# Kernel tuning notes

Hardware: AMD Instinct MI355X
Metric: run time of the kernel (lower is better)

Reference implementation:

```python
import jax, jax.numpy as jnp
import numpy as np

N, C, L = 1024, 3, 6000
CONV_CH = [20, 32, 64, 20]
K = 3            # conv kernel size, padding (K-1)//2 = 1 -> SAME
POOL = 2
HID = 100
FLAT_DIM = (L // POOL**4 + 2 * C + 1) * CONV_CH[-1]  # (375 + 7) * 20 = 7640


def setup_inputs() -> dict:
    key = jax.random.key(0)
    ks = jax.random.split(key, 10)
    d = {"x": jax.random.normal(ks[0], (N, C, L), jnp.float32)}
    ins = [C] + CONV_CH[:-1]
    for i, (ic, oc) in enumerate(zip(ins, CONV_CH)):
        d[f"w{i}"] = jax.random.normal(ks[1 + i], (oc, ic, K), jnp.float32) * (1.0 / np.sqrt(ic * K))
        d[f"b{i}"] = jnp.zeros((oc,), jnp.float32)
    d["wc"] = jax.random.normal(ks[6], (CONV_CH[-1], C, 1), jnp.float32) * (1.0 / np.sqrt(C))
    d["bc"] = jnp.zeros((CONV_CH[-1],), jnp.float32)
    d["wl0"] = jax.random.normal(ks[7], (HID, FLAT_DIM), jnp.float32) * (1.0 / np.sqrt(FLAT_DIM))
    d["bl0"] = jnp.zeros((HID,), jnp.float32)
    d["wl1"] = jax.random.normal(ks[8], (2, HID), jnp.float32) * (1.0 / np.sqrt(HID))
    d["bl1"] = jnp.zeros((2,), jnp.float32)
    return d


def conv1d(x, w, b, pad):
    # x: (N, C_in, L), w: (C_out, C_in, K)
    out = jax.lax.conv_general_dilated(x, w, (1,), [(pad, pad)],
                                       dimension_numbers=('NCH', 'OIH', 'NCH'))
    return out + b[None, :, None]


def maxpool2(x):
    n, c, l = x.shape  # l always even here (6000 / 2^k)
    return x.reshape(n, c, l // 2, 2).max(-1)


def cov_eig_feats(x):
    # batched covariance as a single contraction (avoids the O(N*L*C*C) bmm intermediate)
    n, c, l = x.shape
    diff = x - x.mean(-1, keepdims=True)
    cov = jnp.einsum('ncl,ndl->ncd', diff, diff) / (l - 1)  # (N, C, C)
    # cov is symmetric PSD -> eigh (real); torch uses generic eig and keeps real parts
    vals, vecs = jnp.linalg.eigh(cov)
    vals = vals[..., None] / vals.max()          # global max over batch, like torch
    cov = cov / jnp.abs(cov).max()
    return jnp.concatenate([cov, vals, vecs], axis=-1)  # (N, C, 2C+1)


def reference(x, w0, b0, w1, b1, w2, b2, w3, b3, wc, bc, wl0, bl0, wl1, bl1):
    feats = jax.lax.stop_gradient(cov_eig_feats(x))  # torch branch is @no_grad
    h = x
    for w, b in ((w0, b0), (w1, b1), (w2, b2), (w3, b3)):
        h = maxpool2(jax.nn.relu(conv1d(h, w, b, (K - 1) // 2)))
    h = h.reshape(h.shape[0], -1)                    # (N, 20*375)
    h1 = jax.nn.relu(conv1d(feats, wc, bc, 0))       # (N, 20, 7)
    h1 = h1.reshape(h1.shape[0], -1)
    h = jnp.concatenate([h, h1], axis=1)             # (N, 7640)
    h = jax.nn.relu(h @ wl0.T + bl0)
    out = h @ wl1.T + bl1                            # (N, 2)
    return (out[:, :1], out[:, 1:])
```

## Files before the change

kernel.cpp:

```cpp
#include <hip/hip_runtime.h>
#include <hip/hip_bf16.h>
#include <hip/hip_fp16.h>
#include <math.h>

#define NBATCH 1024
#define LIN    6000
#define HCATW  7640
#define HID    100

#define TCH   54
#define NCHK  7

#define ASZ 3552
#define BSZ 4460

#define W0OFF 0
#define W1OFF 192
#define W2OFF 1472
#define W3OFF 5568
#define B0OFF 9664
#define B1OFF 9684
#define B2OFF 9716
#define B3OFF 9780
#define WREPSZ 9800

#define WL0HSZ (HID * (HCATW/2))

#define FCNS 8

typedef _Float16 v2h __attribute__((ext_vector_type(2)));

__device__ __forceinline__ float fdot2_f16(unsigned int a, unsigned int b, float c) {
#if __has_builtin(__builtin_amdgcn_fdot2)
    v2h ah, bh;
    __builtin_memcpy(&ah, &a, 4);
    __builtin_memcpy(&bh, &b, 4);
    return __builtin_amdgcn_fdot2(ah, bh, c, false);
#else
    float d;
    asm("v_dot2_f32_f16 %0, %1, %2, %3" : "=v"(d) : "v"(a), "v"(b), "v"(c));
    return d;
#endif
}

__device__ __forceinline__ void pack_one(int idx, int OC, int IC, int OCG,
                                         int OPG, int WSTR,
                                         const float* __restrict__ w,
                                         float* __restrict__ dst)
{
    if (idx >= OCG * IC * WSTR) return;
    int ocg = idx / (IC * WSTR);
    int r   = idx - ocg * (IC * WSTR);
    int ic  = r / WSTR;
    int q   = r - ic * WSTR;
    int o   = q / 3, k = q - o * 3;
    int oc  = ocg * OPG + o;
    dst[idx] = (o < OPG && oc < OC) ? w[(oc * IC + ic) * 3 + k] : 0.f;
}

__device__ __forceinline__ void pack_pk(int idx, int OC, int IC, int OCG, int OPG,
                                        const float* __restrict__ w,
                                        unsigned int* __restrict__ dst)
{
    if (idx >= OCG * IC * 16) return;
    int ocg = idx / (IC * 16);
    int r   = idx - ocg * (IC * 16);
    int ic  = r >> 4, q = r & 15;
    int o   = q & 7;
    int oc  = ocg * OPG + o;
    bool valid = (o < OPG) && (oc < OC);
    unsigned int v = 0;
    if (valid) {
        const float* ws = w + (oc * IC + ic) * 3;
        if (q < 8) {
            unsigned int lo = __half_as_ushort(__float2half(ws[0]));
            unsigned int hi = __half_as_ushort(__float2half(ws[1]));
            v = lo | (hi << 16);
        } else {
            v = __float_as_uint(ws[2]);
        }
    }
    dst[idx] = v;
}

__global__ __launch_bounds__(256) void repack_kernel(
    const float* __restrict__ w0, const float* __restrict__ b0,
    const float* __restrict__ w1, const float* __restrict__ b1,
    const float* __restrict__ w2, const float* __restrict__ b2,
    const float* __restrict__ w3, const float* __restrict__ b3,
    float* __restrict__ wrep)
{
    int idx = blockIdx.x * 256 + threadIdx.x;
    unsigned int* wu = (unsigned int*)wrep;
    pack_one(idx, 20,  3, 4, 5, 16, w0, wrep + W0OFF);
    pack_pk (idx, 32, 20, 4, 8, w1, wu + W1OFF);
    pack_pk (idx, 64, 32, 8, 8, w2, wu + W2OFF);
    pack_pk (idx, 20, 64, 4, 5, w3, wu + W3OFF);
    if (idx < 20)            wrep[B0OFF + idx] = b0[idx];
    else if (idx < 52)  { int i = idx - 20;  wrep[B1OFF + i] = b1[i]; }
    else if (idx < 116) { int i = idx - 52;  wrep[B2OFF + i] = b2[i]; }
    else if (idx < 136) { int i = idx - 116; wrep[B3OFF + i] = b3[i]; }
}

__global__ __launch_bounds__(256) void wl0h_kernel(const float* __restrict__ wl0,
                                                   unsigned int* __restrict__ wl0h)
{
    int idx = blockIdx.x * 256 + threadIdx.x;
    if (idx >= WL0HSZ) return;
    float a = wl0[idx * 2], b = wl0[idx * 2 + 1];
    unsigned int lo = __half_as_ushort(__float2half(a));
    unsigned int hi = __half_as_ushort(__float2half(b));
    wl0h[idx] = lo | (hi << 16);
}

template<int IC, int OC, int OCG, int OPG, int WSTR, int JOUT, int LG, int JBLK,
         bool IN16, bool OUT16, bool PKW, bool FINAL>
__device__ __forceinline__ void stage_eo(const float* __restrict__ in,
                                         float* __restrict__ out,
                                         float* __restrict__ outg,
                                         const float* __restrict__ wrep,
                                         const float* __restrict__ brep,
                                         int pbase, int o3, int wv, int lane,
                                         int zero)
{
    constexpr int PIN  = JOUT + 1;
    constexpr int POUT = JOUT / 2;
    constexpr int NJT  = (JOUT + 64 * JBLK - 1) / (64 * JBLK);
    for (int task = wv; task < OCG * NJT; task += 8) {
        const int ocg = task / NJT;
        const int jt  = task - ocg * NJT;
        const int j0  = jt * (64 * JBLK) + lane;
        const float* bp = brep + ocg * OPG;
        float ae[JBLK][OPG], ao[JBLK][OPG];
#pragma unroll
        for (int t = 0; t < JBLK; ++t)
#pragma unroll
            for (int o = 0; o < OPG; ++o) { ae[t][o] = bp[o]; ao[t][o] = ae[t][o]; }
        const float* wbase = wrep + ocg * (IC * WSTR) + zero;
#pragma unroll 2
        for (int ic = 0; ic < IC; ++ic) {
            const float* wp = wbase + ic * WSTR;
            float wr[WSTR];
#pragma unroll
            for (int q = 0; q < WSTR / 4; ++q)
                *(float4*)&wr[q * 4] = *(const float4*)(wp + q * 4);
#pragma unroll
            for (int t = 0; t < JBLK; ++t) {
                const int jj = j0 + t * 64;
                const int jc = (jj < JOUT) ? jj : (JOUT - 1);
                if constexpr (PKW) {
                    const float* ipw = in + ic * PIN;
                    uint2 pw;
                    __builtin_memcpy(&pw, ipw + jc, 8);
                    const unsigned int crossu = (pw.x >> 16) | (pw.y << 16);
                    v2h h1; __builtin_memcpy(&h1, &pw.y, 4);
                    const float e1 = (float)h1.x, o1 = (float)h1.y;
#pragma unroll
                    for (int o = 0; o < OPG; ++o) {
                        const unsigned int wpk = __float_as_uint(wr[o]);
                        const float w2 = wr[8 + o];
                        ae[t][o] = fdot2_f16(pw.x,  wpk, ae[t][o]);
                        ao[t][o] = fdot2_f16(crossu, wpk, ao[t][o]);
                        ae[t][o] = fmaf(e1, w2, ae[t][o]);
                        ao[t][o] = fmaf(o1, w2, ao[t][o]);
                    }
                } else {
                    float e0, e1, o0, o1;
                    if constexpr (IN16) {
                        const float* ipw = in + ic * PIN;
                        uint2 pw;
                        __builtin_memcpy(&pw, ipw + jc, 8);
                        __half2 h0 = *reinterpret_cast<const __half2*>(&pw.x);
                        __half2 h1 = *reinterpret_cast<const __half2*>(&pw.y);
                        e0 = __low2float(h0); o0 = __high2float(h0);
                        e1 = __low2float(h1); o1 = __high2float(h1);
                    } else {
                        const float* ip = in + ic * (2 * PIN);
                        float2 ev, ov;
                        __builtin_memcpy(&ev, ip + jc, 8);
                        __builtin_memcpy(&ov, ip + PIN + jc, 8);
                        e0 = ev.x; e1 = ev.y;
                        o0 = ov.x; o1 = ov.y;
                    }
#pragma unroll
                    for (int o = 0; o < OPG; ++o) {
                        const float w0 = wr[o*3+0], w1 = wr[o*3+1], w2 = wr[o*3+2];
                        ae[t][o] = fmaf(e0, w0, fmaf(o0, w1, fmaf(e1, w2, ae[t][o])));
                        ao[t][o] = fmaf(o0, w0, fmaf(e1, w1, fmaf(o1, w2, ao[t][o])));
                    }
                }
            }
        }
#pragma unroll
        for (int t = 0; t < JBLK; ++t) {
            const int jj = j0 + t * 64;
            if constexpr (FINAL) {
                const int gj = o3 + jj;
                if (gj < 375 && jj < JOUT) {
#pragma unroll
                    for (int o = 0; o < OPG; ++o)
                        outg[(ocg*OPG+o) * 375 + gj] =
                            fmaxf(fmaxf(ae[t][o], ao[t][o]), 0.f);
                }
            } else {
                const int g = pbase + jj;
                const bool val = (jj < JOUT) && (g >= 0) && (g < LG);
                if (jj < JOUT) {
                    if constexpr (OUT16) {
                        __half* dh = (__half*)out;
#pragma unroll
                        for (int o = 0; o < OPG; ++o) {
                            float v = val ? fmaxf(fmaxf(ae[t][o], ao[t][o]), 0.f)
                                          : 0.f;
                            dh[(ocg*OPG+o) * JOUT + jj] = __float2half(v);
                        }
                    } else {
                        float* dst = out + ((jj & 1) ? POUT : 0) + (jj >> 1);
#pragma unroll
                        for (int o = 0; o < OPG; ++o)
                            dst[(ocg*OPG+o) * JOUT] =
                                val ? fmaxf(fmaxf(ae[t][o], ao[t][o]), 0.f) : 0.f;
                    }
                }
            }
        }
    }
}

__device__ __forceinline__ void stage3_split(const float* __restrict__ in,
                                             float* __restrict__ part,
                                             float* __restrict__ outg,
                                             const float* __restrict__ wrep,
                                             const float* __restrict__ brep,
                                             int o3, int wv, int lane, int zero)
{
    constexpr int JOUT = 54, PIND = 55, OPG = 5, WSTR = 16;
    const int ocg = wv & 3, ih = wv >> 2;
    const int j  = lane;
    const int jc = (j < JOUT) ? j : (JOUT - 1);
    const float* bp = brep + ocg * OPG;
    float ae[OPG], ao[OPG];
#pragma unroll
    for (int o = 0; o < OPG; ++o) {
        float b = ih ? 0.f : bp[o];
        ae[o] = b; ao[o] = b;
    }
    const float* wbase = wrep + (ocg * 64 + ih * 32) * WSTR + zero;
#pragma unroll 2
    for (int ic = 0; ic < 32; ++ic) {
        const float* ipw = in + (ih * 32 + ic) * PIND;
        uint2 pw;
        __builtin_memcpy(&pw, ipw + jc, 8);
        const unsigned int crossu = (pw.x >> 16) | (pw.y << 16);
        v2h h1; __builtin_memcpy(&h1, &pw.y, 4);
        const float e1 = (float)h1.x, o1 = (float)h1.y;
        const float* wp = wbase + ic * WSTR;
        float wr[WSTR];
#pragma unroll
        for (int q = 0; q < WSTR / 4; ++q)
            *(float4*)&wr[q * 4] = *(const float4*)(wp + q * 4);
#pragma unroll
        for (int o = 0; o < OPG; ++o) {
            const unsigned int wpk = __float_as_uint(wr[o]);
            const float w2 = wr[8 + o];
            ae[o] = fdot2_f16(pw.x,   wpk, ae[o]);
            ao[o] = fdot2_f16(crossu, wpk, ao[o]);
            ae[o] = fmaf(e1, w2, ae[o]);
            ao[o] = fmaf(o1, w2, ao[o]);
        }
    }
    if (ih == 1) {
#pragma unroll
        for (int o = 0; o < OPG; ++o) {
            float2 p = make_float2(ae[o], ao[o]);
            __builtin_memcpy(part + (ocg * OPG + o) * 128 + lane * 2, &p, 8);
        }
    }
    __syncthreads();
    if (ih == 0) {
#pragma unroll
        for (int o = 0; o < OPG; ++o) {
            float2 p;
            __builtin_memcpy(&p, part + (ocg * OPG + o) * 128 + lane * 2, 8);
            ae[o] += p.x; ao[o] += p.y;
        }
        const int gj = o3 + j;
        if (gj < 375 && j < JOUT) {
#pragma unroll
            for (int o = 0; o < OPG; ++o)
                outg[(ocg * OPG + o) * 375 + gj] =
                    fmaxf(fmaxf(ae[o], ao[o]), 0.f);
        }
    }
}

__global__ __launch_bounds__(512, 8) void conv_chain_eo(
    const float* __restrict__ x,
    const float* __restrict__ wrep,
    float* __restrict__ hcat)
{
    __shared__ float A[ASZ];
    __shared__ float B[BSZ];

    const int tid  = threadIdx.x;
    const int wv   = __builtin_amdgcn_readfirstlane(tid >> 6);
    const int lane = tid & 63;
    const int zero = __builtin_amdgcn_ds_bpermute(0, 0);
    const int n     = blockIdx.x / NCHK;
    const int chunk = blockIdx.x % NCHK;
    const int o3 = chunk * TCH;
    const int p2 = 2*o3 - 1, p1 = 4*o3 - 3, p0 = 8*o3 - 7, xs = 16*o3 - 15;

    const float* xn = x + (size_t)n * 3 * LIN;
    for (int idx = tid; idx < 3 * 894; idx += 512) {
        int c = idx / 894, i = idx - c * 894;
        int g = xs + i;
        float v = (g >= 0 && g < LIN) ? xn[c * LIN + g] : 0.f;
        A[c * 894 + ((i & 1) ? 447 : 0) + (i >> 1)] = v;
    }
    __syncthreads();
    stage_eo< 3, 20, 4, 5, 16, 446, 3000, 2, false, true,  false, false>(
        A, B, nullptr, wrep + W0OFF, wrep + B0OFF, p0, o3, wv, lane, zero);
    __syncthreads();
    stage_eo<20, 32, 4, 8, 16, 222, 1500, 2, true,  true,  true,  false>(
        B, A, nullptr, wrep + W1OFF, wrep + B1OFF, p1, o3, wv, lane, zero);
    __syncthreads();
    stage_eo<32, 64, 8, 8, 16, 110,  750, 2, true,  true,  true,  false>(
        A, B, nullptr, wrep + W2OFF, wrep + B2OFF, p2, o3, wv, lane, zero);
    __syncthreads();
    stage3_split(B, A, hcat + (size_t)n * HCATW,
                 wrep + W3OFF, wrep + B3OFF, o3, wv, lane, zero);
}

__device__ __forceinline__ float fsign(float a, float b) {
    return (b >= 0.0f) ? fabsf(a) : -fabsf(a);
}
__device__ __forceinline__ float slapy2(float xx, float yy) {
    float xa = fabsf(xx), ya = fabsf(yy);
    float w = fmaxf(xa, ya), z = fminf(xa, ya);
    if (z == 0.f) return w;
    float t = z / w;
    return w * sqrtf(1.f + t*t);
}
__device__ __forceinline__ void slartg(float f, float g, float& c, float& s, float& r) {
    if (g == 0.f)      { c = 1.f; s = 0.f; r = f; }
    else if (f == 0.f) { c = 0.f; s = (g >= 0.f ? 1.f : -1.f); r = fabsf(g); }
    else {
        float d = sqrtf(f*f + g*g);
        c = fabsf(f) / d;
        r = fsign(d, f);
        s = g / r;
    }
}
__device__ void slaev2(float a, float b, float cc,
                       float& rt1, float& rt2, float& cs1, float& sn1) {
    float sm = a + cc, df = a - cc;
    float adf = fabsf(df);
    float tb = b + b, ab = fabsf(tb);
    float acmx, acmn;
    if (fabsf(a) > fabsf(cc)) { acmx = a; acmn = cc; } else { acmx = cc; acmn = a; }
    float rt;
    if (adf > ab)      { float t = ab/adf; rt = adf*sqrtf(1.f + t*t); }
    else if (adf < ab) { float t = adf/ab; rt = ab*sqrtf(1.f + t*t); }
    else rt = ab * sqrtf(2.f);
    int sgn1;
    if (sm < 0.f)      { rt1 = 0.5f*(sm - rt); sgn1 = -1; rt2 = (acmx/rt1)*acmn - (b/rt1)*b; }
    else if (sm > 0.f) { rt1 = 0.5f*(sm + rt); sgn1 =  1; rt2 = (acmx/rt1)*acmn - (b/rt1)*b; }
    else               { rt1 = 0.5f*rt; rt2 = -0.5f*rt; sgn1 = 1; }
    float cs; int sgn2;
    if (df >= 0.f) { cs = df + rt; sgn2 = 1; } else { cs = df - rt; sgn2 = -1; }
    float acs = fabsf(cs);
    if (acs > ab) {
        float ct = -tb / cs;
        sn1 = 1.f / sqrtf(1.f + ct*ct);
        cs1 = ct * sn1;
    } else {
        if (ab == 0.f) { cs1 = 1.f; sn1 = 0.f; }
        else {
            float tn = -cs / tb;
            cs1 = 1.f / sqrtf(1.f + tn*tn);
            sn1 = tn * cs1;
        }
    }
    if (sgn1 == sgn2) { float tn = cs1; cs1 = -sn1; sn1 = tn; }
}
__device__ __forceinline__ void rot_cols(float z[3][3], int jc, float c, float s) {
    for (int i = 0; i < 3; ++i) {
        float t = z[i][jc+1];
        z[i][jc+1] = c*t - s*z[i][jc];
        z[i][jc]   = s*t + c*z[i][jc];
    }
}

__device__ void ssteqr3(float d[3], float e[2], float z[3][3]) {
    const float eps    = 5.9604645e-8f;
    const float eps2   = eps * eps;
    const float safmin = 1.17549435e-38f;
    const int n = 3;
    for (int i = 0; i < 3; ++i)
        for (int j = 0; j < 3; ++j) z[i][j] = (i == j) ? 1.f : 0.f;
    const int nmaxit = n * 30;
    int jtot = 0;
    float cw[2], sw[2];
    int l1 = 1, l, m, lend, lsv, lendsv;

L10:
    if (l1 > n) goto L160;
    if (l1 > 1) e[l1-2] = 0.f;
    if (l1 <= n-1) {
        for (m = l1; m <= n-1; ++m) {
            float tst = fabsf(e[m-1]);
            if (tst == 0.f) goto L30;
            if (tst <= (sqrtf(fabsf(d[m-1])) * sqrtf(fabsf(d[m]))) * eps) {
                e[m-1] = 0.f;
                goto L30;
            }
        }
    }
    m = n;
L30:
    l = l1; lsv = l; lend = m; lendsv = lend; l1 = m + 1;
    if (lend == l) goto L10;
    if (fabsf(d[lend-1]) < fabsf(d[l-1])) { lend = lsv; l = lendsv; }
    if (lend > l) {
L40:
        if (l != lend) {
            bool found = false;
            for (m = l; m <= lend-1; ++m) {
                float tst = e[m-1]*e[m-1];
                if (tst <= (eps2*fabsf(d[m-1]))*fabsf(d[m]) + safmin) { found = true; break; }
            }
            if (!found) m = lend;
        } else m = lend;
        if (m < lend) e[m-1] = 0.f;
        {
            float p = d[l-1];
            if (m == l) {
                d[l-1] = p;
                l = l + 1;
                if (l <= lend) goto L40;
                goto L140;
            }
            if (m == l+1) {
                float rt1, rt2, c2, s2;
                slaev2(d[l-1], e[l-1], d[l], rt1, rt2, c2, s2);
                rot_cols(z, l-1, c2, s2);
                d[l-1] = rt1; d[l] = rt2; e[l-1] = 0.f;
                l += 2;
                if (l <= lend) goto L40;
                goto L140;
            }
            if (jtot == nmaxit) goto L140;
            jtot++;
            float g = (d[l] - p) / (2.f * e[l-1]);
            float r = slapy2(g, 1.f);
            g = d[m-1] - p + e[l-1] / (g + fsign(r, g));
            float s = 1.f, c = 1.f;
            p = 0.f;
            for (int i = m-1; i >= l; --i) {
                float f = s * e[i-1];
                float b = c * e[i-1];
                slartg(g, f, c, s, r);
                if (i != m-1) e[i] = r;
                g = d[i] - p;
                r = (d[i-1] - g)*s + 2.f*c*b;
                p = s * r;
                d[i] = g + p;
                g = c*r - b;
                cw[i-l] = c; sw[i-l] = -s;
            }
            for (int jj = m-l; jj >= 1; --jj)
                rot_cols(z, l + jj - 2, cw[jj-1], sw[jj-1]);
            d[l-1] = d[l-1] - p;
            e[l-1] = g;
            goto L40;
        }
    } else {
L90:
        if (l != lend) {
            bool found = false;
            for (m = l; m >= lend+1; --m) {
                float tst = e[m-2]*e[m-2];
                if (tst <= (eps2*fabsf(d[m-1]))*fabsf(d[m-2]) + safmin) { found = true; break; }
            }
            if (!found) m = lend;
        } else m = lend;
        if (m > lend) e[m-2] = 0.f;
        {
            float p = d[l-1];
            if (m == l) {
                d[l-1] = p;
                l = l - 1;
                if (l >= lend) goto L90;
                goto L140;
            }
            if (m == l-1) {
                float rt1, rt2, c2, s2;
                slaev2(d[l-2], e[l-2], d[l-1], rt1, rt2, c2, s2);
                rot_cols(z, l-2, c2, s2);
                d[l-2] = rt1; d[l-1] = rt2; e[l-2] = 0.f;
                l -= 2;
                if (l >= lend) goto L90;
                goto L140;
            }
            if (jtot == nmaxit) goto L140;
            jtot++;
            float g = (d[l-2] - p) / (2.f * e[l-2]);
            float r = slapy2(g, 1.f);
            g = d[m-1] - p + e[l-2] / (g + fsign(r, g));
            float s = 1.f, c = 1.f;
            p = 0.f;
            for (int i = m; i <= l-1; ++i) {
                float f = s * e[i-1];
                float b = c * e[i-1];
                slartg(g, f, c, s, r);
                if (i != m) e[i-2] = r;
                g = d[i-1] - p;
                r = (d[i] - g)*s + 2.f*c*b;
                p = s * r;
                d[i-1] = g + p;
                g = c*r - b;
                cw[i-m] = c; sw[i-m] = s;
            }
            for (int jj = 1; jj <= l-m; ++jj)
                rot_cols(z, m + jj - 2, cw[jj-1], sw[jj-1]);
            d[l-1] = d[l-1] - p;
            e[l-2] = g;
            goto L90;
        }
    }
L140:
    if (jtot < nmaxit) goto L10;
L160:
    for (int ii = 2; ii <= n; ++ii) {
        int i = ii - 1, k = i;
        float p = d[i-1];
        for (int j = ii; j <= n; ++j)
            if (d[j-1] < p) { k = j; p = d[j-1]; }
        if (k != i) {
            d[k-1] = d[i-1]; d[i-1] = p;
            for (int r0 = 0; r0 < 3; ++r0) {
                float t = z[r0][i-1]; z[r0][i-1] = z[r0][k-1]; z[r0][k-1] = t;
            }
        }
    }
}

__global__ __launch_bounds__(256) void cov_eig_kernel(const float* __restrict__ x,
                                                      float* __restrict__ eigbuf,
                                                      unsigned int* __restrict__ gmax)
{
    __shared__ float part[4][9];
    const int n = blockIdx.x;
    const float* xn = x + (size_t)n * 3 * LIN;
    float v[9] = {0,0,0,0,0,0,0,0,0};
    for (int l = threadIdx.x; l < LIN; l += 256) {
        float a = xn[l], b = xn[LIN + l], c = xn[2*LIN + l];
        v[0] += a; v[1] += b; v[2] += c;
        v[3] = fmaf(a,a,v[3]); v[4] = fmaf(a,b,v[4]); v[5] = fmaf(a,c,v[5]);
        v[6] = fmaf(b,b,v[6]); v[7] = fmaf(b,c,v[7]); v[8] = fmaf(c,c,v[8]);
    }
#pragma unroll
    for (int off = 32; off > 0; off >>= 1)
#pragma unroll
        for (int i = 0; i < 9; ++i) v[i] += __shfl_down(v[i], off, 64);
    const int wv = threadIdx.x >> 6, lane = threadIdx.x & 63;
    if (lane == 0)
        for (int i = 0; i < 9; ++i) part[wv][i] = v[i];
    __syncthreads();
    if (threadIdx.x == 0) {
        float t[9];
        for (int i = 0; i < 9; ++i)
            t[i] = part[0][i] + part[1][i] + part[2][i] + part[3][i];
        const float Lf = (float)LIN;
        float m0 = t[0]/Lf, m1 = t[1]/Lf, m2 = t[2]/Lf;
        float c00 = (t[3] - Lf*m0*m0) / (Lf - 1.f);
        float c01 = (t[4] - Lf*m0*m1) / (Lf - 1.f);
        float c02 = (t[5] - Lf*m0*m2) / (Lf - 1.f);
        float c11 = (t[6] - Lf*m1*m1) / (Lf - 1.f);
        float c12 = (t[7] - Lf*m1*m2) / (Lf - 1.f);
        float c22 = (t[8] - Lf*m2*m2) / (Lf - 1.f);

        float dd[3], ee[2], tau, v2;
        {
            float a21 = c01, a31 = c02, a22 = c11, a32 = c12, a33 = c22;
            float xnorm = fabsf(a31);
            if (xnorm == 0.f) {
                tau = 0.f; v2 = 0.f;
                dd[0] = c00; dd[1] = a22; dd[2] = a33;
                ee[0] = a21; ee[1] = a32;
            } else {
                float beta = -fsign(slapy2(a21, xnorm), a21);
                tau = (beta - a21) / beta;
                v2  = a31 / (a21 - beta);
                ee[0] = beta;
                float x1 = tau*(a22 + a32*v2);
                float x2 = tau*(a32 + a33*v2);
                float al = -0.5f*tau*(x1 + x2*v2);
                float w1 = x1 + al;
                float w2 = x2 + al*v2;
                a22 -= 2.f*w1;
                a32 -= (v2*w1 + w2);
                a33 -= 2.f*v2*w2;
                dd[0] = c00; dd[1] = a22; dd[2] = a33;
                ee[1] = a32;
            }
        }
        float zz[3][3];
        ssteqr3(dd, ee, zz);
        if (tau != 0.f) {
            for (int j = 0; j < 3; ++j) {
                float sum = zz[1][j] + v2*zz[2][j];
                zz[1][j] -= tau * sum;
                zz[2][j] -= tau * v2 * sum;
            }
        }

        float* eb = eigbuf + n * 21;
        eb[0] = c00; eb[1] = c01; eb[2] = c02;
        eb[3] = c01; eb[4] = c11; eb[5] = c12;
        eb[6] = c02; eb[7] = c12; eb[8] = c22;
        eb[9] = dd[0]; eb[10] = dd[1]; eb[11] = dd[2];
        for (int c = 0; c < 3; ++c)
            for (int k = 0; k < 3; ++k) eb[12 + c*3 + k] = zz[c][k];

        float vmax = fmaxf(dd[0], fmaxf(dd[1], dd[2]));
        float cmax = 0.f;
        for (int i = 0; i < 9; ++i) cmax = fmaxf(cmax, fabsf(eb[i]));
        atomicMax(&gmax[0], __float_as_uint(vmax));
        atomicMax(&gmax[1], __float_as_uint(cmax));
    }
}

__global__ __launch_bounds__(256) void feats_kernel(const float* __restrict__ eigbuf,
                                                    const unsigned int* __restrict__ gmax,
                                                    const float* __restrict__ wc,
                                                    const float* __restrict__ bc,
                                                    float* __restrict__ hcat)
{
    const int n = blockIdx.x;
    const int t = threadIdx.x;
    if (t >= 140) return;
    const int o = t / 7, j = t % 7;
    const float* eb = eigbuf + n * 21;
    const float vmax = __uint_as_float(gmax[0]);
    const float cmax = __uint_as_float(gmax[1]);
    float f0, f1, f2;
    if (j < 3)       { f0 = eb[0*3+j]/cmax; f1 = eb[1*3+j]/cmax; f2 = eb[2*3+j]/cmax; }
    else if (j == 3) { f0 = eb[9]/vmax;     f1 = eb[10]/vmax;    f2 = eb[11]/vmax; }
    else             { int k = j-4; f0 = eb[12+0*3+k]; f1 = eb[12+1*3+k]; f2 = eb[12+2*3+k]; }
    float r = bc[o] + wc[o*3+0]*f0 + wc[o*3+1]*f1 + wc[o*3+2]*f2;
    hcat[(size_t)n*HCATW + 7500 + o*7 + j] = fmaxf(r, 0.f);
}

__global__ __launch_bounds__(512) void fc01_kernel(const float* __restrict__ hcat,
                                                   const unsigned int* __restrict__ wl0h,
                                                   const float* __restrict__ bl0,
                                                   const float* __restrict__ wl1,
                                                   const float* __restrict__ bl1,
                                                   float* __restrict__ out)
{
    __shared__ __half hl[FCNS * HCATW];
    __shared__ float hbuf[FCNS * HID];
    const int tid = threadIdx.x;
    const int n0 = blockIdx.x * FCNS;
    for (int i = tid; i < FCNS * (HCATW/4); i += 512) {
        int s  = i / (HCATW/4);
        int k4 = i - s * (HCATW/4);
        float4 v = *(const float4*)(hcat + (size_t)(n0 + s) * HCATW + k4 * 4);
        __half2 h01 = __floats2half2_rn(v.x, v.y);
        __half2 h23 = __floats2half2_rn(v.z, v.w);
        *(__half2*)(hl + s * HCATW + k4 * 4)     = h01;
        *(__half2*)(hl + s * HCATW + k4 * 4 + 2) = h23;
    }
    __syncthreads();
    const int wv = tid >> 6;
    const int lane = tid & 63;
    for (int ot = wv; ot < HID / 4; ot += 8) {
        float acc[4][FCNS];
#pragma unroll
        for (int oo = 0; oo < 4; ++oo)
#pragma unroll
            for (int s = 0; s < FCNS; ++s) acc[oo][s] = 0.f;
        for (int k = lane * 8; k < HCATW; k += 512) {
            uint4 hv[FCNS];
#pragma unroll
            for (int s = 0; s < FCNS; ++s)
                hv[s] = *(const uint4*)(hl + s * HCATW + k);
#pragma unroll
            for (int oo = 0; oo < 4; ++oo) {
                const uint4 wp = *(const uint4*)(wl0h + (ot*4+oo) * (HCATW/2) + (k >> 1));
#pragma unroll
                for (int s = 0; s < FCNS; ++s) {
                    float a = acc[oo][s];
                    a = fdot2_f16(hv[s].x, wp.x, a);
                    a = fdot2_f16(hv[s].y, wp.y, a);
                    a = fdot2_f16(hv[s].z, wp.z, a);
                    a = fdot2_f16(hv[s].w, wp.w, a);
                    acc[oo][s] = a;
                }
            }
        }
#pragma unroll
        for (int off = 32; off > 0; off >>= 1)
#pragma unroll
            for (int oo = 0; oo < 4; ++oo)
#pragma unroll
                for (int s = 0; s < FCNS; ++s)
                    acc[oo][s] += __shfl_down(acc[oo][s], off, 64);
        if (lane == 0) {
#pragma unroll
            for (int oo = 0; oo < 4; ++oo) {
                const float b = bl0[ot*4+oo];
#pragma unroll
                for (int s = 0; s < FCNS; ++s)
                    hbuf[s * HID + ot*4+oo] = fmaxf(acc[oo][s] + b, 0.f);
            }
        }
    }
    __syncthreads();
    if (tid < 2 * FCNS) {
        const int s = tid >> 1, r = tid & 1;
        const float* w = wl1 + r * HID;
        float acc = bl1[r];
        for (int k = 0; k < HID; ++k) acc = fmaf(hbuf[s * HID + k], w[k], acc);
        out[r * NBATCH + n0 + s] = acc;
    }
}

extern "C" void kernel_launch(void* const* d_in, const int* in_sizes, int n_in,
                              void* d_out, int out_size, void* d_ws, size_t ws_size,
                              hipStream_t stream)
{
    const float* x   = (const float*)d_in[0];
    const float* w0  = (const float*)d_in[1];
    const float* b0  = (const float*)d_in[2];
    const float* w1  = (const float*)d_in[3];
    const float* b1  = (const float*)d_in[4];
    const float* w2  = (const float*)d_in[5];
    const float* b2  = (const float*)d_in[6];
    const float* w3  = (const float*)d_in[7];
    const float* b3  = (const float*)d_in[8];
    const float* wc  = (const float*)d_in[9];
    const float* bc  = (const float*)d_in[10];
    const float* wl0 = (const float*)d_in[11];
    const float* bl0 = (const float*)d_in[12];
    const float* wl1 = (const float*)d_in[13];
    const float* bl1 = (const float*)d_in[14];
    float* out = (float*)d_out;

    const size_t HCAT_N = (size_t)NBATCH * HCATW;
    const size_t EIG_N  = (size_t)NBATCH * 21;
    const size_t need_bytes = (HCAT_N + EIG_N + 4 + WREPSZ + WL0HSZ) * 4 + 16;
    if (ws_size < need_bytes) return;

    float* ws     = (float*)d_ws;
    float* hcat   = ws;
    float* eigbuf = hcat + HCAT_N;
    unsigned int* gmax = (unsigned int*)(eigbuf + EIG_N);
    float* wrep   = (float*)(gmax + 4);
    unsigned int* wl0h = (unsigned int*)(wrep + WREPSZ);

    hipMemsetAsync(gmax, 0, 2 * sizeof(unsigned int), stream);

    repack_kernel<<<16, 256, 0, stream>>>(w0, b0, w1, b1, w2, b2, w3, b3, wrep);
    wl0h_kernel<<<(WL0HSZ + 255) / 256, 256, 0, stream>>>(wl0, wl0h);
    conv_chain_eo<<<NBATCH * NCHK, 512, 0, stream>>>(x, wrep, hcat);
    cov_eig_kernel<<<NBATCH, 256, 0, stream>>>(x, eigbuf, gmax);
    feats_kernel<<<NBATCH, 256, 0, stream>>>(eigbuf, gmax, wc, bc, hcat);
    fc01_kernel<<<NBATCH / FCNS, 512, 0, stream>>>(hcat, wl0h, bl0, wl1, bl1, out);
}
```

Baseline: 615.4 us.

## Use packed fp16 FMA accumulation for conv stages 1-2 and merge prep kernels

Conv stages 1 and 2 now accumulate in packed half2 registers using hfma2, with weights repacked as duplicated fp16 pairs (stride 24). This replaces the previous dot2 plus fp32 FMA mix. The aim is to cut ALU instruction count in the dominant conv kernel. Two smaller changes come with it: the weight-repack and wl0 fp16 conversion kernels are merged into one launch, and the covariance reduction uses float4 loads. The cost is that accumulation happens in fp16, which risks precision loss and overflow over 20-32 input channels.

Result: no change. 610.1 us (-0.9%).

```diff
diff --git a/kernel.cpp b/kernel.cpp
--- a/kernel.cpp
+++ b/kernel.cpp
@@ -1,5 +1,4 @@
 #include <hip/hip_runtime.h>
-#include <hip/hip_bf16.h>
 #include <hip/hip_fp16.h>
 #include <math.h>
 
@@ -16,13 +15,13 @@
 
 #define W0OFF 0
 #define W1OFF 192
-#define W2OFF 1472
-#define W3OFF 5568
-#define B0OFF 9664
-#define B1OFF 9684
-#define B2OFF 9716
-#define B3OFF 9780
-#define WREPSZ 9800
+#define W2OFF 2112
+#define W3OFF 8256
+#define B0OFF 12352
+#define B1OFF 12372
+#define B2OFF 12404
+#define B3OFF 12468
+#define WREPSZ 12496
 
 #define WL0HSZ (HID * (HCATW/2))
 
@@ -43,6 +42,10 @@
 #endif
 }
 
+__device__ __forceinline__ __half2 u2h2(unsigned int u) {
+    __half2 h; __builtin_memcpy(&h, &u, 4); return h;
+}
+
 __device__ __forceinline__ void pack_one(int idx, int OC, int IC, int OCG,
                                          int OPG, int WSTR,
                                          const float* __restrict__ w,
@@ -56,6 +59,22 @@
     int o   = q / 3, k = q - o * 3;
     int oc  = ocg * OPG + o;
     dst[idx] = (o < OPG && oc < OC) ? w[(oc * IC + ic) * 3 + k] : 0.f;
+}
+
+__device__ __forceinline__ void pack_pk16(int idx, int OC, int IC,
+                                          const float* __restrict__ w,
+                                          unsigned int* __restrict__ dst)
+{
+    const int OCG = OC >> 3;
+    if (idx >= OCG * IC * 24) return;
+    int ocg = idx / (IC * 24);
+    int r   = idx - ocg * (IC * 24);
+    int ic  = r / 24, q = r - ic * 24;
+    int o   = q / 3, k = q - o * 3;
+    int oc  = ocg * 8 + o;
+    float wv = w[(oc * IC + ic) * 3 + k];
+    unsigned int h = __half_as_ushort(__float2half(wv));
+    dst[idx] = h | (h << 16);
 }
 
 __device__ __forceinline__ void pack_pk(int idx, int OC, int IC, int OCG, int OPG,
@@ -83,38 +102,36 @@
     dst[idx] = v;
 }
 
-__global__ __launch_bounds__(256) void repack_kernel(
+__global__ __launch_bounds__(256) void prep_kernel(
     const float* __restrict__ w0, const float* __restrict__ b0,
     const float* __restrict__ w1, const float* __restrict__ b1,
     const float* __restrict__ w2, const float* __restrict__ b2,
     const float* __restrict__ w3, const float* __restrict__ b3,
-    float* __restrict__ wrep)
+    const float* __restrict__ wl0,
+    float* __restrict__ wrep, unsigned int* __restrict__ wl0h)
 {
     int idx = blockIdx.x * 256 + threadIdx.x;
-    unsigned int* wu = (unsigned int*)wrep;
-    pack_one(idx, 20,  3, 4, 5, 16, w0, wrep + W0OFF);
-    pack_pk (idx, 32, 20, 4, 8, w1, wu + W1OFF);
-    pack_pk (idx, 64, 32, 8, 8, w2, wu + W2OFF);
-    pack_pk (idx, 20, 64, 4, 5, w3, wu + W3OFF);
-    if (idx < 20)            wrep[B0OFF + idx] = b0[idx];
-    else if (idx < 52)  { int i = idx - 20;  wrep[B1OFF + i] = b1[i]; }
-    else if (idx < 116) { int i = idx - 52;  wrep[B2OFF + i] = b2[i]; }
-    else if (idx < 136) { int i = idx - 116; wrep[B3OFF + i] = b3[i]; }
-}
-
-__global__ __launch_bounds__(256) void wl0h_kernel(const float* __restrict__ wl0,
-                                                   unsigned int* __restrict__ wl0h)
-{
-    int idx = blockIdx.x * 256 + threadIdx.x;
-    if (idx >= WL0HSZ) return;
-    float a = wl0[idx * 2], b = wl0[idx * 2 + 1];
-    unsigned int lo = __half_as_ushort(__float2half(a));
-    unsigned int hi = __half_as_ushort(__float2half(b));
-    wl0h[idx] = lo | (hi << 16);
+    if (idx < WL0HSZ) {
+        float a = wl0[idx * 2], b = wl0[idx * 2 + 1];
+        unsigned int lo = __half_as_ushort(__float2half(a));
+        unsigned int hi = __half_as_ushort(__float2half(b));
+        wl0h[idx] = lo | (hi << 16);
+    }
+    if (idx < 8192) {
+        unsigned int* wu = (unsigned int*)wrep;
+        pack_one (idx, 20,  3, 4, 5, 16, w0, wrep + W0OFF);
+        pack_pk16(idx, 32, 20, w1, wu + W1OFF);
+        pack_pk16(idx, 64, 32, w2, wu + W2OFF);
+        pack_pk  (idx, 20, 64, 4, 5, w3, wu + W3OFF);
+        if (idx < 20)            wrep[B0OFF + idx] = b0[idx];
+        else if (idx < 52)  { int i = idx - 20;  wrep[B1OFF + i] = b1[i]; }
+        else if (idx < 116) { int i = idx - 52;  wrep[B2OFF + i] = b2[i]; }
+        else if (idx < 136) { int i = idx - 116; wrep[B3OFF + i] = b3[i]; }
+    }
 }
 
 template<int IC, int OC, int OCG, int OPG, int WSTR, int JOUT, int LG, int JBLK,
-         bool IN16, bool OUT16, bool PKW, bool FINAL>
+         bool IN16, bool OUT16, bool PK16, bool FINAL>
 __device__ __forceinline__ void stage_eo(const float* __restrict__ in,
                                          float* __restrict__ out,
                                          float* __restrict__ outg,
@@ -132,13 +149,24 @@
         const int j0  = jt * (64 * JBLK) + lane;
         const float* bp = brep + ocg * OPG;
         float ae[JBLK][OPG], ao[JBLK][OPG];
-#pragma unroll
-        for (int t = 0; t < JBLK; ++t)
-#pragma unroll
-            for (int o = 0; o < OPG; ++o) { ae[t][o] = bp[o]; ao[t][o] = ae[t][o]; }
+        __half2 ap[JBLK][OPG];
+        if constexpr (PK16) {
+#pragma unroll
+            for (int t = 0; t < JBLK; ++t)
+#pragma unroll
+                for (int o = 0; o < OPG; ++o) {
+                    __half hb = __float2half(bp[o]);
+                    ap[t][o] = __halves2half2(hb, hb);
+                }
+        } else {
+#pragma unroll
+            for (int t = 0; t < JBLK; ++t)
+#pragma unroll
+                for (int o = 0; o < OPG; ++o) { ae[t][o] = bp[o]; ao[t][o] = ae[t][o]; }
+        }
         const float* wbase = wrep + ocg * (IC * WSTR) + zero;
-#pragma unroll 2
-        for (int ic = 0; ic < IC; ++ic) {
+
+        auto icbody = [&](int ic) {
             const float* wp = wbase + ic * WSTR;
             float wr[WSTR];
 #pragma unroll
@@ -148,21 +176,18 @@
             for (int t = 0; t < JBLK; ++t) {
                 const int jj = j0 + t * 64;
                 const int jc = (jj < JOUT) ? jj : (JOUT - 1);
-                if constexpr (PKW) {
+                if constexpr (PK16) {
                     const float* ipw = in + ic * PIN;
                     uint2 pw;
                     __builtin_memcpy(&pw, ipw + jc, 8);
                     const unsigned int crossu = (pw.x >> 16) | (pw.y << 16);
-                    v2h h1; __builtin_memcpy(&h1, &pw.y, 4);
-                    const float e1 = (float)h1.x, o1 = (float)h1.y;
 #pragma unroll
                     for (int o = 0; o < OPG; ++o) {
-                        const unsigned int wpk = __float_as_uint(wr[o]);
-                        const float w2 = wr[8 + o];
-                        ae[t][o] = fdot2_f16(pw.x,  wpk, ae[t][o]);
-                        ao[t][o] = fdot2_f16(crossu, wpk, ao[t][o]);
-                        ae[t][o] = fmaf(e1, w2, ae[t][o]);
-                        ao[t][o] = fmaf(o1, w2, ao[t][o]);
+                        __half2 a = ap[t][o];
+                        a = __hfma2(u2h2(pw.x),   u2h2(__float_as_uint(wr[o*3+0])), a);
+                        a = __hfma2(u2h2(crossu), u2h2(__float_as_uint(wr[o*3+1])), a);
+                        a = __hfma2(u2h2(pw.y),   u2h2(__float_as_uint(wr[o*3+2])), a);
+                        ap[t][o] = a;
                     }
                 } else {
                     float e0, e1, o0, o1;
@@ -170,8 +195,8 @@
                         const float* ipw = in + ic * PIN;
                         uint2 pw;
                         __builtin_memcpy(&pw, ipw + jc, 8);
-                        __half2 h0 = *reinterpret_cast<const __half2*>(&pw.x);
-                        __half2 h1 = *reinterpret_cast<const __half2*>(&pw.y);
+                        __half2 h0 = u2h2(pw.x);
+                        __half2 h1 = u2h2(pw.y);
                         e0 = __low2float(h0); o0 = __high2float(h0);
                         e1 = __low2float(h1); o1 = __high2float(h1);
                     } else {
@@ -190,7 +215,15 @@
                     }
                 }
             }
-        }
+        };
+        if constexpr (PK16) {
+#pragma unroll 1
+            for (int ic = 0; ic < IC; ++ic) icbody(ic);
+        } else {
+#pragma unroll 2
+            for (int ic = 0; ic < IC; ++ic) icbody(ic);
+        }
+
 #pragma unroll
         for (int t = 0; t < JBLK; ++t) {
             const int jj = j0 + t * 64;
@@ -206,7 +239,16 @@
                 const int g = pbase + jj;
                 const bool val = (jj < JOUT) && (g >= 0) && (g < LG);
                 if (jj < JOUT) {
-                    if constexpr (OUT16) {
+                    if constexpr (PK16) {
+                        __half* dh = (__half*)out;
+#pragma unroll
+                        for (int o = 0; o < OPG; ++o) {
+                            float ee = __low2float(ap[t][o]);
+                            float oo = __high2float(ap[t][o]);
+                            float v = val ? fmaxf(fmaxf(ee, oo), 0.f) : 0.f;
+                            dh[(ocg*OPG+o) * JOUT + jj] = __float2half(v);
+                        }
+                    } else if constexpr (OUT16) {
                         __half* dh = (__half*)out;
 #pragma unroll
                         for (int o = 0; o < OPG; ++o) {
@@ -322,10 +364,10 @@
     stage_eo< 3, 20, 4, 5, 16, 446, 3000, 2, false, true,  false, false>(
         A, B, nullptr, wrep + W0OFF, wrep + B0OFF, p0, o3, wv, lane, zero);
     __syncthreads();
-    stage_eo<20, 32, 4, 8, 16, 222, 1500, 2, true,  true,  true,  false>(
+    stage_eo<20, 32, 4, 8, 24, 222, 1500, 2, true,  true,  true,  false>(
         B, A, nullptr, wrep + W1OFF, wrep + B1OFF, p1, o3, wv, lane, zero);
     __syncthreads();
-    stage_eo<32, 64, 8, 8, 16, 110,  750, 2, true,  true,  true,  false>(
+    stage_eo<32, 64, 8, 8, 24, 110,  750, 2, true,  true,  true,  false>(
         A, B, nullptr, wrep + W2OFF, wrep + B2OFF, p2, o3, wv, lane, zero);
     __syncthreads();
     stage3_split(B, A, hcat + (size_t)n * HCATW,
@@ -554,11 +596,19 @@
     const int n = blockIdx.x;
     const float* xn = x + (size_t)n * 3 * LIN;
     float v[9] = {0,0,0,0,0,0,0,0,0};
-    for (int l = threadIdx.x; l < LIN; l += 256) {
-        float a = xn[l], b = xn[LIN + l], c = xn[2*LIN + l];
-        v[0] += a; v[1] += b; v[2] += c;
-        v[3] = fmaf(a,a,v[3]); v[4] = fmaf(a,b,v[4]); v[5] = fmaf(a,c,v[5]);
-        v[6] = fmaf(b,b,v[6]); v[7] = fmaf(b,c,v[7]); v[8] = fmaf(c,c,v[8]);
+    for (int i = threadIdx.x; i < LIN / 4; i += 256) {
+        float4 a = *(const float4*)(xn + 4 * i);
+        float4 b = *(const float4*)(xn + LIN + 4 * i);
+        float4 c = *(const float4*)(xn + 2 * LIN + 4 * i);
+        v[0] += (a.x + a.y) + (a.z + a.w);
+        v[1] += (b.x + b.y) + (b.z + b.w);
+        v[2] += (c.x + c.y) + (c.z + c.w);
+        v[3] = fmaf(a.x,a.x, fmaf(a.y,a.y, fmaf(a.z,a.z, fmaf(a.w,a.w, v[3]))));
+        v[4] = fmaf(a.x,b.x, fmaf(a.y,b.y, fmaf(a.z,b.z, fmaf(a.w,b.w, v[4]))));
+        v[5] = fmaf(a.x,c.x, fmaf(a.y,c.y, fmaf(a.z,c.z, fmaf(a.w,c.w, v[5]))));
+        v[6] = fmaf(b.x,b.x, fmaf(b.y,b.y, fmaf(b.z,b.z, fmaf(b.w,b.w, v[6]))));
+        v[7] = fmaf(b.x,c.x, fmaf(b.y,c.y, fmaf(b.z,c.z, fmaf(b.w,c.w, v[7]))));
+        v[8] = fmaf(c.x,c.x, fmaf(c.y,c.y, fmaf(c.z,c.z, fmaf(c.w,c.w, v[8]))));
     }
 #pragma unroll
     for (int off = 32; off > 0; off >>= 1)
@@ -763,8 +813,8 @@
 
     hipMemsetAsync(gmax, 0, 2 * sizeof(unsigned int), stream);
 
-    repack_kernel<<<16, 256, 0, stream>>>(w0, b0, w1, b1, w2, b2, w3, b3, wrep);
-    wl0h_kernel<<<(WL0HSZ + 255) / 256, 256, 0, stream>>>(wl0, wl0h);
+    prep_kernel<<<(WL0HSZ + 255) / 256, 256, 0, stream>>>(
+        w0, b0, w1, b1, w2, b2, w3, b3, wl0, wrep, wl0h);
     conv_chain_eo<<<NBATCH * NCHK, 512, 0, stream>>>(x, wrep, hcat);
     cov_eig_kernel<<<NBATCH, 256, 0, stream>>>(x, eigbuf, gmax);
     feats_kernel<<<NBATCH, 256, 0, stream>>>(eigbuf, gmax, wc, bc, hcat);
```
